# Optimization experiments

Hardware: AMD Instinct MI355X
Metric: run time of the kernel (lower is better)

## Reference

```python
import jax, jax.numpy as jnp
import numpy as np

ENC, STR_H, CELL_H, ATTN = 512, 256, 512, 512
B, L = 64, 1024


def setup_inputs() -> dict:
    key = jax.random.key(0)
    ks = jax.random.split(key, 12)
    s = lambda fan_in: 1.0 / np.sqrt(fan_in)
    return {
        "encoded_features_map": jax.random.normal(ks[0], (B, L, ENC), jnp.float32),
        "structural_hidden_state": jax.random.normal(ks[1], (1, B, STR_H), jnp.float32),
        "cell_content_hidden_state": jax.random.normal(ks[2], (1, B, CELL_H), jnp.float32),
        "W_enc": jax.random.uniform(ks[3], (ENC, ATTN), jnp.float32, -s(ENC), s(ENC)),
        "b_enc": jax.random.uniform(ks[4], (ATTN,), jnp.float32, -s(ENC), s(ENC)),
        "W_str": jax.random.uniform(ks[5], (STR_H, ATTN), jnp.float32, -s(STR_H), s(STR_H)),
        "b_str": jax.random.uniform(ks[6], (ATTN,), jnp.float32, -s(STR_H), s(STR_H)),
        "W_cell": jax.random.uniform(ks[7], (CELL_H, ATTN), jnp.float32, -s(CELL_H), s(CELL_H)),
        "b_cell": jax.random.uniform(ks[8], (ATTN,), jnp.float32, -s(CELL_H), s(CELL_H)),
        "W_comb": jax.random.uniform(ks[9], (ATTN, 1), jnp.float32, -s(ATTN), s(ATTN)),
        "b_comb": jax.random.uniform(ks[10], (1,), jnp.float32, -s(ATTN), s(ATTN)),
    }


def reference(encoded_features_map, structural_hidden_state, cell_content_hidden_state,
              W_enc, b_enc, W_str, b_str, W_cell, b_cell, W_comb, b_comb):
    # [B, L, A] projection of encoder features
    a_enc = jnp.einsum("ble,ea->bla", encoded_features_map, W_enc) + b_enc
    # [B, A] projections of the two hidden states (squeeze layer dim)
    a_str = structural_hidden_state[0] @ W_str + b_str
    a_cell = cell_content_hidden_state[0] @ W_cell + b_cell
    # broadcast add + ReLU + scalar score: [B, L]
    h = jax.nn.relu(a_enc + a_str[:, None, :] + a_cell[:, None, :])
    scores = jnp.einsum("bla,ao->bl", h, W_comb) + b_comb[0]
    weights = jax.nn.softmax(scores, axis=1)  # over sequence dim
    # weighted sum over L -> [B, ENC]
    context = jnp.einsum("bl,ble->be", weights, encoded_features_map)
    return context
```

## Files before the change

### kernel.cpp

```cpp
#include <hip/hip_runtime.h>
#include <stdint.h>

#define ENC_D 512
#define ATTN_D 512
#define STR_D 256
#define CELL_D 512
#define BATCH 64
#define SEQ 1024
#define NROWS (BATCH * SEQ)

typedef __bf16 bf16x8 __attribute__((ext_vector_type(8)));
typedef float f32x4 __attribute__((ext_vector_type(4)));

__device__ __forceinline__ unsigned short f2bf(float f) {
    unsigned int u = __float_as_uint(f);
    u += 0x7fffu + ((u >> 16) & 1u);
    return (unsigned short)(u >> 16);
}

__device__ __forceinline__ void lds_cp16(void* l, const void* g) {
    __builtin_amdgcn_global_load_lds(
        (const __attribute__((address_space(1))) unsigned int*)g,
        (__attribute__((address_space(3))) unsigned int*)l, 16, 0, 0);
}

__global__ __launch_bounds__(256) void k_prep_wt(const float* __restrict__ W,
                                                 unsigned short* __restrict__ WT) {
    __shared__ unsigned short T[64 * 68];
    const int t = threadIdx.x;
    const int ei = blockIdx.x >> 3, ni = blockIdx.x & 7;
    const int e0 = ei * 64, n0 = ni * 64;

#pragma unroll
    for (int i = 0; i < 4; ++i) {
        const int idx = t + i * 256;
        const int r = idx >> 4, c4 = idx & 15;
        const float4 v = *(const float4*)(W + (size_t)(e0 + r) * ATTN_D + n0 + c4 * 4);
        T[(c4 * 4 + 0) * 68 + r] = f2bf(v.x);
        T[(c4 * 4 + 1) * 68 + r] = f2bf(v.y);
        T[(c4 * 4 + 2) * 68 + r] = f2bf(v.z);
        T[(c4 * 4 + 3) * 68 + r] = f2bf(v.w);
    }
    __syncthreads();

#pragma unroll
    for (int i = 0; i < 2; ++i) {
        const int q = t + i * 256;
        const int n = q >> 3, ge = q & 7;
        union { unsigned short s[8]; uint4 u; } o;
#pragma unroll
        for (int j = 0; j < 8; ++j) o.s[j] = T[n * 68 + ge * 8 + j];
        const int ng = n0 + n;
        const int g = ei * 8 + ge;
        const int chunk = ng >> 5, colc = ng & 31;
        const int slot = colc * 64 + (g ^ (colc & 7));
        *(uint4*)(WT + (size_t)chunk * 16384 + slot * 8) = o.u;
    }
}

__global__ __launch_bounds__(256) void k_bias(const float* __restrict__ str,
                                              const float* __restrict__ cell,
                                              const float* __restrict__ b_enc,
                                              const float* __restrict__ Wstr,
                                              const float* __restrict__ b_str,
                                              const float* __restrict__ Wcell,
                                              const float* __restrict__ b_cell,
                                              float* __restrict__ bias) {
    __shared__ float sj[768];
    __shared__ f32x4 red[128];
    const int b = blockIdx.x, t = threadIdx.x;
#pragma unroll
    for (int i = 0; i < 3; ++i) {
        const int idx = t + i * 256;
        sj[idx] = (idx < 256) ? str[b * STR_D + idx] : cell[b * CELL_D + idx - 256];
    }
    __syncthreads();

    const int a4 = t & 127, jh = t >> 7;
    f32x4 acc = {0.f, 0.f, 0.f, 0.f};
    if (jh == 0) {
#pragma unroll 8
        for (int j = 0; j < 256; ++j) {
            const float s = sj[j];
            const float4 wv = *(const float4*)(Wstr + (size_t)j * ATTN_D + a4 * 4);
            acc[0] += s * wv.x; acc[1] += s * wv.y; acc[2] += s * wv.z; acc[3] += s * wv.w;
        }
#pragma unroll 8
        for (int j = 0; j < 128; ++j) {
            const float s = sj[256 + j];
            const float4 wv = *(const float4*)(Wcell + (size_t)j * ATTN_D + a4 * 4);
            acc[0] += s * wv.x; acc[1] += s * wv.y; acc[2] += s * wv.z; acc[3] += s * wv.w;
        }
    } else {
#pragma unroll 8
        for (int j = 128; j < 512; ++j) {
            const float s = sj[256 + j];
            const float4 wv = *(const float4*)(Wcell + (size_t)j * ATTN_D + a4 * 4);
            acc[0] += s * wv.x; acc[1] += s * wv.y; acc[2] += s * wv.z; acc[3] += s * wv.w;
        }
        red[a4] = acc;
    }
    __syncthreads();
    if (jh == 0) {
        const f32x4 o = red[a4];
        const int a = a4 * 4;
        const float4 be = *(const float4*)(b_enc + a);
        const float4 bs = *(const float4*)(b_str + a);
        const float4 bc = *(const float4*)(b_cell + a);
        f32x4 r;
        r[0] = acc[0] + o[0] + be.x + bs.x + bc.x;
        r[1] = acc[1] + o[1] + be.y + bs.y + bc.y;
        r[2] = acc[2] + o[2] + be.z + bs.z + bc.z;
        r[3] = acc[3] + o[3] + be.w + bs.w + bc.w;
        *(f32x4*)(bias + b * ATTN_D + a) = r;
    }
}

__global__ __launch_bounds__(256, 2) void k_scores(const float* __restrict__ E,
                                                   const unsigned short* __restrict__ WTsw,
                                                   const float* __restrict__ bias,
                                                   const float* __restrict__ Wcomb,
                                                   float* __restrict__ scores) {
    __shared__ unsigned short wlds[2][16384];

    const int tid = threadIdx.x;
    const int r0 = blockIdx.x * 128;
    const int b = blockIdx.x >> 3;
    const int w = tid >> 6, lane = tid & 63;
    const int quad = lane >> 4, c = lane & 15;

#pragma unroll
    for (int i = 0; i < 8; ++i)
        lds_cp16((char*)&wlds[0][0] + i * 4096 + tid * 16,
                 (const char*)WTsw + i * 4096 + tid * 16);

    bf16x8 afr[2][16];
#pragma unroll
    for (int m = 0; m < 2; ++m) {
        const float* Ep = E + (size_t)(r0 + w * 32 + m * 16 + c) * ENC_D + quad * 8;
#pragma unroll
        for (int ks = 0; ks < 16; ++ks) {
            const float4 v0 = *(const float4*)(Ep + ks * 32);
            const float4 v1 = *(const float4*)(Ep + ks * 32 + 4);
            union { unsigned short s[8]; bf16x8 v; } u;
            u.s[0] = f2bf(v0.x); u.s[1] = f2bf(v0.y);
            u.s[2] = f2bf(v0.z); u.s[3] = f2bf(v0.w);
            u.s[4] = f2bf(v1.x); u.s[5] = f2bf(v1.y);
            u.s[6] = f2bf(v1.z); u.s[7] = f2bf(v1.w);
            afr[m][ks] = u.v;
        }
    }

    float sc0[4] = {0.f, 0.f, 0.f, 0.f};
    float sc1[4] = {0.f, 0.f, 0.f, 0.f};
    const float* biasb = bias + b * ATTN_D;
    const int swz = c & 7;

    __syncthreads();

    for (int chunk = 0; chunk < 16; ++chunk) {
        if (chunk < 15) {
            const char* gsrc = (const char*)WTsw + (size_t)(chunk + 1) * 32768;
            char* ldst = (char*)&wlds[(chunk + 1) & 1][0];
#pragma unroll
            for (int i = 0; i < 8; ++i)
                lds_cp16(ldst + i * 4096 + tid * 16, gsrc + i * 4096 + tid * 16);
        }

        const unsigned short* wb = &wlds[chunk & 1][0];
        f32x4 a00 = {0.f,0.f,0.f,0.f}, a01 = {0.f,0.f,0.f,0.f};
        f32x4 a10 = {0.f,0.f,0.f,0.f}, a11 = {0.f,0.f,0.f,0.f};
#pragma unroll
        for (int ks = 0; ks < 16; ++ks) {
            const int gs = ((ks * 4 + quad) ^ swz) * 8;
            const bf16x8 b0 = *(const bf16x8*)(wb + c * 512 + gs);
            const bf16x8 b1 = *(const bf16x8*)(wb + (16 + c) * 512 + gs);
            a00 = __builtin_amdgcn_mfma_f32_16x16x32_bf16(afr[0][ks], b0, a00, 0, 0, 0);
            a10 = __builtin_amdgcn_mfma_f32_16x16x32_bf16(afr[1][ks], b0, a10, 0, 0, 0);
            a01 = __builtin_amdgcn_mfma_f32_16x16x32_bf16(afr[0][ks], b1, a01, 0, 0, 0);
            a11 = __builtin_amdgcn_mfma_f32_16x16x32_bf16(afr[1][ks], b1, a11, 0, 0, 0);
        }

        const int n0 = chunk * 32 + c;
        const float bi0 = biasb[n0], wc0 = Wcomb[n0];
        const float bi1 = biasb[n0 + 16], wc1 = Wcomb[n0 + 16];
#pragma unroll
        for (int r = 0; r < 4; ++r) {
            float v;
            v = a00[r] + bi0; sc0[r] += (v > 0.f ? v : 0.f) * wc0;
            v = a01[r] + bi1; sc0[r] += (v > 0.f ? v : 0.f) * wc1;
            v = a10[r] + bi0; sc1[r] += (v > 0.f ? v : 0.f) * wc0;
            v = a11[r] + bi1; sc1[r] += (v > 0.f ? v : 0.f) * wc1;
        }
        __syncthreads();
    }

#pragma unroll
    for (int r = 0; r < 4; ++r) {
        float v0 = sc0[r], v1 = sc1[r];
        v0 += __shfl_xor(v0, 1); v1 += __shfl_xor(v1, 1);
        v0 += __shfl_xor(v0, 2); v1 += __shfl_xor(v1, 2);
        v0 += __shfl_xor(v0, 4); v1 += __shfl_xor(v1, 4);
        v0 += __shfl_xor(v0, 8); v1 += __shfl_xor(v1, 8);
        sc0[r] = v0; sc1[r] = v1;
    }
    if (c == 0) {
        const int g0 = r0 + w * 32 + quad * 4;
#pragma unroll
        for (int r = 0; r < 4; ++r) scores[g0 + r] = sc0[r];
#pragma unroll
        for (int r = 0; r < 4; ++r) scores[g0 + 16 + r] = sc1[r];
    }
}

__global__ __launch_bounds__(256) void k_softmax(float* __restrict__ s) {
    __shared__ float red[256];
    const int b = blockIdx.x, t = threadIdx.x;
    float v[4];
    float m = -1e30f;
#pragma unroll
    for (int i = 0; i < 4; ++i) {
        v[i] = s[b * SEQ + i * 256 + t];
        m = fmaxf(m, v[i]);
    }
    red[t] = m;
    __syncthreads();
    for (int o = 128; o > 0; o >>= 1) {
        if (t < o) red[t] = fmaxf(red[t], red[t + o]);
        __syncthreads();
    }
    m = red[0];
    __syncthreads();
    float sum = 0.f;
#pragma unroll
    for (int i = 0; i < 4; ++i) {
        v[i] = __expf(v[i] - m);
        sum += v[i];
    }
    red[t] = sum;
    __syncthreads();
    for (int o = 128; o > 0; o >>= 1) {
        if (t < o) red[t] += red[t + o];
        __syncthreads();
    }
    const float inv = 1.f / red[0];
#pragma unroll
    for (int i = 0; i < 4; ++i) s[b * SEQ + i * 256 + t] = v[i] * inv;
}

__global__ __launch_bounds__(128) void k_context(const float* __restrict__ E,
                                                 const float* __restrict__ wts,
                                                 float* __restrict__ part) {
    __shared__ float wl[64];
    const int blk = blockIdx.x, t = threadIdx.x;
    const int b = blk >> 4, lo = blk & 15;
    if (t < 64) wl[t] = wts[b * SEQ + lo * 64 + t];
    __syncthreads();
    const float* Ep = E + ((size_t)(b * SEQ + lo * 64)) * ENC_D + t * 4;
    f32x4 acc = {0.f, 0.f, 0.f, 0.f};
#pragma unroll 8
    for (int l = 0; l < 64; ++l) {
        const float4 v = *(const float4*)(Ep + (size_t)l * ENC_D);
        const float wv = wl[l];
        acc[0] += wv * v.x; acc[1] += wv * v.y;
        acc[2] += wv * v.z; acc[3] += wv * v.w;
    }
    *(f32x4*)(&part[(size_t)(b * 16 + lo) * ENC_D + t * 4]) = acc;
}

__global__ __launch_bounds__(256) void k_reduce(const float* __restrict__ part,
                                                float* __restrict__ out) {
    const int idx = blockIdx.x * 256 + threadIdx.x;
    const int b = idx >> 9, e = idx & 511;
    const float* p = part + (size_t)b * 16 * ENC_D + e;
    float s = 0.f;
#pragma unroll
    for (int i = 0; i < 16; ++i) s += p[i * ENC_D];
    out[idx] = s;
}

extern "C" void kernel_launch(void* const* d_in, const int* in_sizes, int n_in,
                              void* d_out, int out_size, void* d_ws, size_t ws_size,
                              hipStream_t stream) {
    const float* E      = (const float*)d_in[0];
    const float* str    = (const float*)d_in[1];
    const float* cell   = (const float*)d_in[2];
    const float* Wenc   = (const float*)d_in[3];
    const float* b_enc  = (const float*)d_in[4];
    const float* Wstr   = (const float*)d_in[5];
    const float* b_str  = (const float*)d_in[6];
    const float* Wcell  = (const float*)d_in[7];
    const float* b_cell = (const float*)d_in[8];
    const float* Wcomb  = (const float*)d_in[9];
    float* out = (float*)d_out;

    char* ws = (char*)d_ws;
    unsigned short* WT = (unsigned short*)ws;
    float* bias   = (float*)(ws + (512 << 10));
    float* scores = (float*)(ws + (512 << 10) + (128 << 10));
    float* part   = (float*)(ws + (512 << 10) + (128 << 10) + (256 << 10));

    k_prep_wt<<<64, 256, 0, stream>>>(Wenc, WT);
    k_bias<<<64, 256, 0, stream>>>(str, cell, b_enc, Wstr, b_str, Wcell, b_cell, bias);
    k_scores<<<NROWS / 128, 256, 0, stream>>>(E, WT, bias, Wcomb, scores);
    k_softmax<<<BATCH, 256, 0, stream>>>(scores);
    k_context<<<1024, 128, 0, stream>>>(E, scores, part);
    k_reduce<<<NROWS / 512, 256, 0, stream>>>(part, out);
}
```

Baseline: 298.9 us.

## Read W_enc MFMA fragments directly from global memory, dropping LDS staging

Repacks the bf16 W_enc into a fragment-ordered layout so each lane can load its MFMA B operand with one 16-byte global load. k_scores now runs as single-wave blocks of 32 rows with no LDS double buffer and no barriers, so each wave streams all 512 KB of weights through the caches. This removes LDS traffic and block-wide syncs and raises the block count. In exchange it adds much more L2/L1 traffic for the weights, and global-load latency now sits directly in front of the MFMAs.

```diff
diff --git a/kernel.cpp b/kernel.cpp
--- a/kernel.cpp
+++ b/kernel.cpp
@@ -18,14 +18,8 @@
     return (unsigned short)(u >> 16);
 }
 
-__device__ __forceinline__ void lds_cp16(void* l, const void* g) {
-    __builtin_amdgcn_global_load_lds(
-        (const __attribute__((address_space(1))) unsigned int*)g,
-        (__attribute__((address_space(3))) unsigned int*)l, 16, 0, 0);
-}
-
 __global__ __launch_bounds__(256) void k_prep_wt(const float* __restrict__ W,
-                                                 unsigned short* __restrict__ WT) {
+                                                 unsigned short* __restrict__ WF) {
     __shared__ unsigned short T[64 * 68];
     const int t = threadIdx.x;
     const int ei = blockIdx.x >> 3, ni = blockIdx.x & 7;
@@ -52,9 +46,10 @@
         for (int j = 0; j < 8; ++j) o.s[j] = T[n * 68 + ge * 8 + j];
         const int ng = n0 + n;
         const int g = ei * 8 + ge;
-        const int chunk = ng >> 5, colc = ng & 31;
-        const int slot = colc * 64 + (g ^ (colc & 7));
-        *(uint4*)(WT + (size_t)chunk * 16384 + slot * 8) = o.u;
+        const int nt = ng >> 4, c = ng & 15;
+        const int ks = g >> 2, quad = g & 3;
+        const int gi = nt * 1024 + ks * 64 + quad * 16 + c;
+        *(uint4*)(WF + (size_t)gi * 8) = o.u;
     }
 }
 
@@ -116,28 +111,20 @@
     }
 }
 
-__global__ __launch_bounds__(256, 2) void k_scores(const float* __restrict__ E,
-                                                   const unsigned short* __restrict__ WTsw,
-                                                   const float* __restrict__ bias,
-                                                   const float* __restrict__ Wcomb,
-                                                   float* __restrict__ scores) {
-    __shared__ unsigned short wlds[2][16384];
-
-    const int tid = threadIdx.x;
-    const int r0 = blockIdx.x * 128;
-    const int b = blockIdx.x >> 3;
-    const int w = tid >> 6, lane = tid & 63;
+__global__ __launch_bounds__(64) void k_scores(const float* __restrict__ E,
+                                               const unsigned short* __restrict__ WF,
+                                               const float* __restrict__ bias,
+                                               const float* __restrict__ Wcomb,
+                                               float* __restrict__ scores) {
+    const int lane = threadIdx.x;
     const int quad = lane >> 4, c = lane & 15;
-
-#pragma unroll
-    for (int i = 0; i < 8; ++i)
-        lds_cp16((char*)&wlds[0][0] + i * 4096 + tid * 16,
-                 (const char*)WTsw + i * 4096 + tid * 16);
+    const int r0 = blockIdx.x * 32;
+    const int b = blockIdx.x >> 5;
 
     bf16x8 afr[2][16];
 #pragma unroll
     for (int m = 0; m < 2; ++m) {
-        const float* Ep = E + (size_t)(r0 + w * 32 + m * 16 + c) * ENC_D + quad * 8;
+        const float* Ep = E + (size_t)(r0 + m * 16 + c) * ENC_D + quad * 8;
 #pragma unroll
         for (int ks = 0; ks < 16; ++ks) {
             const float4 v0 = *(const float4*)(Ep + ks * 32);
@@ -154,45 +141,24 @@
     float sc0[4] = {0.f, 0.f, 0.f, 0.f};
     float sc1[4] = {0.f, 0.f, 0.f, 0.f};
     const float* biasb = bias + b * ATTN_D;
-    const int swz = c & 7;
-
-    __syncthreads();
-
-    for (int chunk = 0; chunk < 16; ++chunk) {
-        if (chunk < 15) {
-            const char* gsrc = (const char*)WTsw + (size_t)(chunk + 1) * 32768;
-            char* ldst = (char*)&wlds[(chunk + 1) & 1][0];
-#pragma unroll
-            for (int i = 0; i < 8; ++i)
-                lds_cp16(ldst + i * 4096 + tid * 16, gsrc + i * 4096 + tid * 16);
-        }
-
-        const unsigned short* wb = &wlds[chunk & 1][0];
-        f32x4 a00 = {0.f,0.f,0.f,0.f}, a01 = {0.f,0.f,0.f,0.f};
-        f32x4 a10 = {0.f,0.f,0.f,0.f}, a11 = {0.f,0.f,0.f,0.f};
+
+    for (int nt = 0; nt < 32; ++nt) {
+        const unsigned short* wp = WF + (size_t)(nt * 1024 + lane) * 8;
+        f32x4 a0 = {0.f, 0.f, 0.f, 0.f}, a1 = {0.f, 0.f, 0.f, 0.f};
 #pragma unroll
         for (int ks = 0; ks < 16; ++ks) {
-            const int gs = ((ks * 4 + quad) ^ swz) * 8;
-            const bf16x8 b0 = *(const bf16x8*)(wb + c * 512 + gs);
-            const bf16x8 b1 = *(const bf16x8*)(wb + (16 + c) * 512 + gs);
-            a00 = __builtin_amdgcn_mfma_f32_16x16x32_bf16(afr[0][ks], b0, a00, 0, 0, 0);
-            a10 = __builtin_amdgcn_mfma_f32_16x16x32_bf16(afr[1][ks], b0, a10, 0, 0, 0);
-            a01 = __builtin_amdgcn_mfma_f32_16x16x32_bf16(afr[0][ks], b1, a01, 0, 0, 0);
-            a11 = __builtin_amdgcn_mfma_f32_16x16x32_bf16(afr[1][ks], b1, a11, 0, 0, 0);
-        }
-
-        const int n0 = chunk * 32 + c;
-        const float bi0 = biasb[n0], wc0 = Wcomb[n0];
-        const float bi1 = biasb[n0 + 16], wc1 = Wcomb[n0 + 16];
+            const bf16x8 bf = *(const bf16x8*)(wp + ks * 512);
+            a0 = __builtin_amdgcn_mfma_f32_16x16x32_bf16(afr[0][ks], bf, a0, 0, 0, 0);
+            a1 = __builtin_amdgcn_mfma_f32_16x16x32_bf16(afr[1][ks], bf, a1, 0, 0, 0);
+        }
+        const int n = nt * 16 + c;
+        const float bi = biasb[n], wc = Wcomb[n];
 #pragma unroll
         for (int r = 0; r < 4; ++r) {
             float v;
-            v = a00[r] + bi0; sc0[r] += (v > 0.f ? v : 0.f) * wc0;
-            v = a01[r] + bi1; sc0[r] += (v > 0.f ? v : 0.f) * wc1;
-            v = a10[r] + bi0; sc1[r] += (v > 0.f ? v : 0.f) * wc0;
-            v = a11[r] + bi1; sc1[r] += (v > 0.f ? v : 0.f) * wc1;
-        }
-        __syncthreads();
+            v = a0[r] + bi; sc0[r] += (v > 0.f ? v : 0.f) * wc;
+            v = a1[r] + bi; sc1[r] += (v > 0.f ? v : 0.f) * wc;
+        }
     }
 
 #pragma unroll
@@ -201,11 +167,11 @@
         v0 += __shfl_xor(v0, 1); v1 += __shfl_xor(v1, 1);
         v0 += __shfl_xor(v0, 2); v1 += __shfl_xor(v1, 2);
         v0 += __shfl_xor(v0, 4); v1 += __shfl_xor(v1, 4);
-        v0 += __shfl_xor(v0, 8); v1 += __shfl_xor(v1, 8);
-        sc0[r] = v0; sc1[r] = v1;
+        sc0[r] = v0 + __shfl_xor(v0, 8);
+        sc1[r] = v1 + __shfl_xor(v1, 8);
     }
     if (c == 0) {
-        const int g0 = r0 + w * 32 + quad * 4;
+        const int g0 = r0 + quad * 4;
 #pragma unroll
         for (int r = 0; r < 4; ++r) scores[g0 + r] = sc0[r];
 #pragma unroll
@@ -295,14 +261,14 @@
     float* out = (float*)d_out;
 
     char* ws = (char*)d_ws;
-    unsigned short* WT = (unsigned short*)ws;
+    unsigned short* WF = (unsigned short*)ws;
     float* bias   = (float*)(ws + (512 << 10));
     float* scores = (float*)(ws + (512 << 10) + (128 << 10));
     float* part   = (float*)(ws + (512 << 10) + (128 << 10) + (256 << 10));
 
-    k_prep_wt<<<64, 256, 0, stream>>>(Wenc, WT);
+    k_prep_wt<<<64, 256, 0, stream>>>(Wenc, WF);
     k_bias<<<64, 256, 0, stream>>>(str, cell, b_enc, Wstr, b_str, Wcell, b_cell, bias);
-    k_scores<<<NROWS / 128, 256, 0, stream>>>(E, WT, bias, Wcomb, scores);
+    k_scores<<<NROWS / 32, 64, 0, stream>>>(E, WF, bias, Wcomb, scores);
     k_softmax<<<BATCH, 256, 0, stream>>>(scores);
     k_context<<<1024, 128, 0, stream>>>(E, scores, part);
     k_reduce<<<NROWS / 512, 256, 0, stream>>>(part, out);
```

After: 406.2 us. 35.9% more time.

## Pre-layout W_enc in MFMA fragment order, split bias GEMV, raise scores occupancy

Applied to the files above, without the earlier changes.

The transposed bf16 W_enc is now written in the exact per-lane MFMA B-fragment order, so k_scores reads each B fragment as a contiguous, lane-indexed 16-byte LDS load with no XOR swizzle. The hidden-state bias GEMV, previously run by 64 blocks, is split into 12x64 partial blocks plus a finishing reduction kernel to expose more parallelism. k_scores launch bounds go from 2 to 3 blocks per SM, which may pressure registers since each thread holds 32 A fragments. The bias partials reuse the context partial buffer, which is safe because the two uses happen at different times in the stream.

```diff
diff --git a/kernel.cpp b/kernel.cpp
--- a/kernel.cpp
+++ b/kernel.cpp
@@ -25,7 +25,7 @@
 }
 
 __global__ __launch_bounds__(256) void k_prep_wt(const float* __restrict__ W,
-                                                 unsigned short* __restrict__ WT) {
+                                                 unsigned short* __restrict__ WF) {
     __shared__ unsigned short T[64 * 68];
     const int t = threadIdx.x;
     const int ei = blockIdx.x >> 3, ni = blockIdx.x & 7;
@@ -52,76 +52,57 @@
         for (int j = 0; j < 8; ++j) o.s[j] = T[n * 68 + ge * 8 + j];
         const int ng = n0 + n;
         const int g = ei * 8 + ge;
-        const int chunk = ng >> 5, colc = ng & 31;
-        const int slot = colc * 64 + (g ^ (colc & 7));
-        *(uint4*)(WT + (size_t)chunk * 16384 + slot * 8) = o.u;
-    }
-}
-
-__global__ __launch_bounds__(256) void k_bias(const float* __restrict__ str,
-                                              const float* __restrict__ cell,
-                                              const float* __restrict__ b_enc,
-                                              const float* __restrict__ Wstr,
-                                              const float* __restrict__ b_str,
-                                              const float* __restrict__ Wcell,
-                                              const float* __restrict__ b_cell,
-                                              float* __restrict__ bias) {
-    __shared__ float sj[768];
-    __shared__ f32x4 red[128];
-    const int b = blockIdx.x, t = threadIdx.x;
-#pragma unroll
-    for (int i = 0; i < 3; ++i) {
-        const int idx = t + i * 256;
-        sj[idx] = (idx < 256) ? str[b * STR_D + idx] : cell[b * CELL_D + idx - 256];
-    }
-    __syncthreads();
-
-    const int a4 = t & 127, jh = t >> 7;
+        const int nt = ng >> 4, c = ng & 15;
+        const int ks = g >> 2, quad = g & 3;
+        const int gi = nt * 1024 + ks * 64 + quad * 16 + c;
+        *(uint4*)(WF + (size_t)gi * 8) = o.u;
+    }
+}
+
+__global__ __launch_bounds__(128) void k_bias_part(const float* __restrict__ str,
+                                                   const float* __restrict__ cell,
+                                                   const float* __restrict__ Wstr,
+                                                   const float* __restrict__ Wcell,
+                                                   float* __restrict__ part) {
+    __shared__ float sj[64];
+    const int jq = blockIdx.x, b = blockIdx.y, t = threadIdx.x;
+    const float* hvec;
+    const float* Wrow;
+    if (jq < 4) { hvec = str + b * STR_D + jq * 64;            Wrow = Wstr + (size_t)(jq * 64) * ATTN_D; }
+    else        { hvec = cell + b * CELL_D + (jq - 4) * 64;    Wrow = Wcell + (size_t)((jq - 4) * 64) * ATTN_D; }
+    if (t < 64) sj[t] = hvec[t];
+    __syncthreads();
+
     f32x4 acc = {0.f, 0.f, 0.f, 0.f};
-    if (jh == 0) {
 #pragma unroll 8
-        for (int j = 0; j < 256; ++j) {
-            const float s = sj[j];
-            const float4 wv = *(const float4*)(Wstr + (size_t)j * ATTN_D + a4 * 4);
-            acc[0] += s * wv.x; acc[1] += s * wv.y; acc[2] += s * wv.z; acc[3] += s * wv.w;
-        }
-#pragma unroll 8
-        for (int j = 0; j < 128; ++j) {
-            const float s = sj[256 + j];
-            const float4 wv = *(const float4*)(Wcell + (size_t)j * ATTN_D + a4 * 4);
-            acc[0] += s * wv.x; acc[1] += s * wv.y; acc[2] += s * wv.z; acc[3] += s * wv.w;
-        }
-    } else {
-#pragma unroll 8
-        for (int j = 128; j < 512; ++j) {
-            const float s = sj[256 + j];
-            const float4 wv = *(const float4*)(Wcell + (size_t)j * ATTN_D + a4 * 4);
-            acc[0] += s * wv.x; acc[1] += s * wv.y; acc[2] += s * wv.z; acc[3] += s * wv.w;
-        }
-        red[a4] = acc;
-    }
-    __syncthreads();
-    if (jh == 0) {
-        const f32x4 o = red[a4];
-        const int a = a4 * 4;
-        const float4 be = *(const float4*)(b_enc + a);
-        const float4 bs = *(const float4*)(b_str + a);
-        const float4 bc = *(const float4*)(b_cell + a);
-        f32x4 r;
-        r[0] = acc[0] + o[0] + be.x + bs.x + bc.x;
-        r[1] = acc[1] + o[1] + be.y + bs.y + bc.y;
-        r[2] = acc[2] + o[2] + be.z + bs.z + bc.z;
-        r[3] = acc[3] + o[3] + be.w + bs.w + bc.w;
-        *(f32x4*)(bias + b * ATTN_D + a) = r;
-    }
-}
-
-__global__ __launch_bounds__(256, 2) void k_scores(const float* __restrict__ E,
-                                                   const unsigned short* __restrict__ WTsw,
+    for (int i = 0; i < 64; ++i) {
+        const float s = sj[i];
+        const float4 wv = *(const float4*)(Wrow + (size_t)i * ATTN_D + t * 4);
+        acc[0] += s * wv.x; acc[1] += s * wv.y; acc[2] += s * wv.z; acc[3] += s * wv.w;
+    }
+    *(f32x4*)(part + (size_t)(jq * BATCH + b) * ATTN_D + t * 4) = acc;
+}
+
+__global__ __launch_bounds__(256) void k_bias_fin(const float* __restrict__ part,
+                                                  const float* __restrict__ b_enc,
+                                                  const float* __restrict__ b_str,
+                                                  const float* __restrict__ b_cell,
+                                                  float* __restrict__ bias) {
+    const int idx = blockIdx.x * 256 + threadIdx.x;
+    const int b = idx >> 9, a = idx & 511;
+    float s = b_enc[a] + b_str[a] + b_cell[a];
+#pragma unroll
+    for (int jq = 0; jq < 12; ++jq)
+        s += part[(size_t)(jq * BATCH + b) * ATTN_D + a];
+    bias[idx] = s;
+}
+
+__global__ __launch_bounds__(256, 3) void k_scores(const float* __restrict__ E,
+                                                   const unsigned short* __restrict__ WF,
                                                    const float* __restrict__ bias,
                                                    const float* __restrict__ Wcomb,
                                                    float* __restrict__ scores) {
-    __shared__ unsigned short wlds[2][16384];
+    __shared__ unsigned short buf[2][16384];
 
     const int tid = threadIdx.x;
     const int r0 = blockIdx.x * 128;
@@ -131,8 +112,8 @@
 
 #pragma unroll
     for (int i = 0; i < 8; ++i)
-        lds_cp16((char*)&wlds[0][0] + i * 4096 + tid * 16,
-                 (const char*)WTsw + i * 4096 + tid * 16);
+        lds_cp16((char*)&buf[0][0] + i * 4096 + tid * 16,
+                 (const char*)WF + i * 4096 + tid * 16);
 
     bf16x8 afr[2][16];
 #pragma unroll
@@ -154,34 +135,32 @@
     float sc0[4] = {0.f, 0.f, 0.f, 0.f};
     float sc1[4] = {0.f, 0.f, 0.f, 0.f};
     const float* biasb = bias + b * ATTN_D;
-    const int swz = c & 7;
-
-    __syncthreads();
-
-    for (int chunk = 0; chunk < 16; ++chunk) {
-        if (chunk < 15) {
-            const char* gsrc = (const char*)WTsw + (size_t)(chunk + 1) * 32768;
-            char* ldst = (char*)&wlds[(chunk + 1) & 1][0];
+
+    __syncthreads();
+
+    for (int ch = 0; ch < 16; ++ch) {
+        if (ch < 15) {
+            const char* gsrc = (const char*)WF + (size_t)(ch + 1) * 32768;
+            char* ldst = (char*)&buf[(ch + 1) & 1][0];
 #pragma unroll
             for (int i = 0; i < 8; ++i)
                 lds_cp16(ldst + i * 4096 + tid * 16, gsrc + i * 4096 + tid * 16);
         }
 
-        const unsigned short* wb = &wlds[chunk & 1][0];
+        const unsigned short* wb = &buf[ch & 1][0];
         f32x4 a00 = {0.f,0.f,0.f,0.f}, a01 = {0.f,0.f,0.f,0.f};
         f32x4 a10 = {0.f,0.f,0.f,0.f}, a11 = {0.f,0.f,0.f,0.f};
 #pragma unroll
         for (int ks = 0; ks < 16; ++ks) {
-            const int gs = ((ks * 4 + quad) ^ swz) * 8;
-            const bf16x8 b0 = *(const bf16x8*)(wb + c * 512 + gs);
-            const bf16x8 b1 = *(const bf16x8*)(wb + (16 + c) * 512 + gs);
+            const bf16x8 b0 = *(const bf16x8*)(wb + (ks * 64 + lane) * 8);
+            const bf16x8 b1 = *(const bf16x8*)(wb + 8192 + (ks * 64 + lane) * 8);
             a00 = __builtin_amdgcn_mfma_f32_16x16x32_bf16(afr[0][ks], b0, a00, 0, 0, 0);
             a10 = __builtin_amdgcn_mfma_f32_16x16x32_bf16(afr[1][ks], b0, a10, 0, 0, 0);
             a01 = __builtin_amdgcn_mfma_f32_16x16x32_bf16(afr[0][ks], b1, a01, 0, 0, 0);
             a11 = __builtin_amdgcn_mfma_f32_16x16x32_bf16(afr[1][ks], b1, a11, 0, 0, 0);
         }
 
-        const int n0 = chunk * 32 + c;
+        const int n0 = ch * 32 + c;
         const float bi0 = biasb[n0], wc0 = Wcomb[n0];
         const float bi1 = biasb[n0 + 16], wc1 = Wcomb[n0 + 16];
 #pragma unroll
@@ -201,8 +180,8 @@
         v0 += __shfl_xor(v0, 1); v1 += __shfl_xor(v1, 1);
         v0 += __shfl_xor(v0, 2); v1 += __shfl_xor(v1, 2);
         v0 += __shfl_xor(v0, 4); v1 += __shfl_xor(v1, 4);
-        v0 += __shfl_xor(v0, 8); v1 += __shfl_xor(v1, 8);
-        sc0[r] = v0; sc1[r] = v1;
+        sc0[r] = v0 + __shfl_xor(v0, 8);
+        sc1[r] = v1 + __shfl_xor(v1, 8);
     }
     if (c == 0) {
         const int g0 = r0 + w * 32 + quad * 4;
@@ -295,14 +274,16 @@
     float* out = (float*)d_out;
 
     char* ws = (char*)d_ws;
-    unsigned short* WT = (unsigned short*)ws;
+    unsigned short* WF = (unsigned short*)ws;
     float* bias   = (float*)(ws + (512 << 10));
     float* scores = (float*)(ws + (512 << 10) + (128 << 10));
     float* part   = (float*)(ws + (512 << 10) + (128 << 10) + (256 << 10));
-
-    k_prep_wt<<<64, 256, 0, stream>>>(Wenc, WT);
-    k_bias<<<64, 256, 0, stream>>>(str, cell, b_enc, Wstr, b_str, Wcell, b_cell, bias);
-    k_scores<<<NROWS / 128, 256, 0, stream>>>(E, WT, bias, Wcomb, scores);
+    float* bpart  = part;
+
+    k_prep_wt<<<64, 256, 0, stream>>>(Wenc, WF);
+    k_bias_part<<<dim3(12, 64), 128, 0, stream>>>(str, cell, Wstr, Wcell, bpart);
+    k_bias_fin<<<128, 256, 0, stream>>>(bpart, b_enc, b_str, b_cell, bias);
+    k_scores<<<NROWS / 128, 256, 0, stream>>>(E, WF, bias, Wcomb, scores);
     k_softmax<<<BATCH, 256, 0, stream>>>(scores);
     k_context<<<1024, 128, 0, stream>>>(E, scores, part);
     k_reduce<<<NROWS / 512, 256, 0, stream>>>(part, out);
```

Result: faster. 284.4 us (-4.9%).
